# Kernel tuning notes

Measured on AMD Instinct MI355X. Metric: run time of the kernel, lower is better.

Reference implementation:

```python
import jax, jax.numpy as jnp
import numpy as np

# --- static problem geometry (compile-time constants, as in MinkowskiEngine decompositions) ---
N_TOTAL = 500000          # total points across all clouds
C = 128                   # feature channels
G = 32                    # GroupNorm groups
EPS = 1e-5                # torch GroupNorm default
LENGTHS = np.array([40000, 55000, 70000, 45000, 80000, 65000, 90000, 55000])  # points per cloud
assert LENGTHS.sum() == N_TOTAL
B = len(LENGTHS)
SEG = np.repeat(np.arange(B), LENGTHS)  # [N] cloud id for each position of the concatenated permutation


def setup_inputs() -> dict:
    key = jax.random.key(0)
    k1, k2, k3, k4 = jax.random.split(key, 4)
    feats = jax.random.normal(k1, (N_TOTAL, C), dtype=jnp.float32)   # x.F
    # concatenated decomposition_permutations: a permutation of arange(N)
    perm = jax.random.permutation(k2, N_TOTAL).astype(jnp.int64)
    gamma = 1.0 + 0.1 * jax.random.normal(k3, (C,), dtype=jnp.float32)  # GroupNorm weight
    beta = 0.1 * jax.random.normal(k4, (C,), dtype=jnp.float32)         # GroupNorm bias
    return {"feats": feats, "gamma": gamma, "beta": beta, "perm": perm}


def reference(feats, gamma, beta, perm):
    Cg = C // G
    seg = jnp.asarray(SEG)                              # [N]
    x = feats[perm]                                     # [N, C] per-cloud gather (concatenated)
    xg = x.reshape(-1, G, Cg)                           # [N, G, Cg]
    # per-(cloud, group) statistics over all points of the cloud and channels of the group
    s = jax.ops.segment_sum(xg.sum(-1), seg, num_segments=B)            # [B, G]
    ss = jax.ops.segment_sum((xg * xg).sum(-1), seg, num_segments=B)    # [B, G]
    cnt = jnp.asarray(LENGTHS * Cg, dtype=feats.dtype)[:, None]          # [B, 1]
    mean = s / cnt
    var = ss / cnt - mean * mean
    inv = jax.lax.rsqrt(var + EPS)                      # [B, G]
    xn = (xg - mean[seg][:, :, None]) * inv[seg][:, :, None]             # [N, G, Cg]
    y = xn.reshape(-1, C) * gamma + beta                # [N, C] affine per channel
    # scatter back via inverse permutation: out[perm[i]] = y[i]
    out = jnp.zeros_like(y).at[perm].set(y)
    return out
```

## Files before the change

kernel.cpp:

```cpp
#include <hip/hip_runtime.h>

#define N_TOTAL 500000
#define C 128
#define G 32
#define NB 8
#define EPS 1e-5f
#define NBLK 2048
#define RPB ((N_TOTAL + NBLK - 1) / NBLK)

typedef float f4 __attribute__((ext_vector_type(4)));

__device__ __forceinline__ int cloud_of(int i) {
    int c = 0;
    c += (i >= 40000);
    c += (i >= 95000);
    c += (i >= 165000);
    c += (i >= 210000);
    c += (i >= 290000);
    c += (i >= 355000);
    c += (i >= 445000);
    return c;
}

__device__ const float d_cnt[NB] = {160000.f, 220000.f, 280000.f, 180000.f,
                                    320000.f, 260000.f, 360000.f, 220000.f};


__global__ __launch_bounds__(256) void gn_prep(const int* __restrict__ perm,
                                               unsigned char* __restrict__ cid,
                                               float* __restrict__ ws) {
    int gid = blockIdx.x * 256 + threadIdx.x;
    if (gid < 2 * NB * G) ws[gid] = 0.f;
    for (int i = gid; i < N_TOTAL; i += 512 * 256)
        cid[perm[i]] = (unsigned char)cloud_of(i);
}

#define ACCUM(v, cl)                                                          \
    do {                                                                      \
        float rs_ = (v).x + (v).y + (v).z + (v).w;                            \
        float rss_ = (v).x * (v).x + (v).y * (v).y + (v).z * (v).z +          \
                     (v).w * (v).w;                                           \
        _Pragma("unroll")                                                     \
        for (int b = 0; b < NB; b++)                                          \
            if ((cl) == b) { s[b] += rs_; ss[b] += rss_; }                    \
    } while (0)

__global__ __launch_bounds__(256) void gn_stats(const float* __restrict__ feats,
                                                const unsigned char* __restrict__ cid,
                                                float* __restrict__ ws) {
    __shared__ float lacc[2 * NB * G];
    int tid = threadIdx.x;
    for (int k = tid; k < 2 * NB * G; k += 256) lacc[k] = 0.f;
    __syncthreads();

    const int g = tid & 31;
    const int rsub = tid >> 5;
    int start = blockIdx.x * RPB;
    int end = start + RPB;
    if (end > N_TOTAL) end = N_TOTAL;

    float s[NB], ss[NB];
#pragma unroll
    for (int b = 0; b < NB; b++) { s[b] = 0.f; ss[b] = 0.f; }

    int row = start + rsub;
    for (; row + 24 < end; row += 32) {
        int c0 = cid[row], c1 = cid[row + 8], c2 = cid[row + 16], c3 = cid[row + 24];
        f4 v0 = ((const f4*)(feats + ((long long)(row)      << 7)))[g];
        f4 v1 = ((const f4*)(feats + ((long long)(row + 8)  << 7)))[g];
        f4 v2 = ((const f4*)(feats + ((long long)(row + 16) << 7)))[g];
        f4 v3 = ((const f4*)(feats + ((long long)(row + 24) << 7)))[g];
        ACCUM(v0, c0); ACCUM(v1, c1); ACCUM(v2, c2); ACCUM(v3, c3);
    }
    for (; row < end; row += 8) {
        int c0 = cid[row];
        f4 v0 = ((const f4*)(feats + ((long long)row << 7)))[g];
        ACCUM(v0, c0);
    }

#pragma unroll
    for (int b = 0; b < NB; b++) {
        if (s[b] != 0.f || ss[b] != 0.f) {
            atomicAdd(&lacc[b * G + g], s[b]);
            atomicAdd(&lacc[NB * G + b * G + g], ss[b]);
        }
    }
    __syncthreads();

    for (int k = tid; k < 2 * NB * G; k += 256) {
        float a = lacc[k];
        if (a != 0.f) atomicAdd(&ws[k], a);
    }
}

__global__ __launch_bounds__(256) void gn_apply(const float* __restrict__ feats,
                                                const unsigned char* __restrict__ cid,
                                                const float* __restrict__ gamma,
                                                const float* __restrict__ beta,
                                                const float* __restrict__ ws,
                                                float* __restrict__ out) {
    __shared__ float lmean[NB * G];
    __shared__ float linv[NB * G];
    int tid = threadIdx.x;
    {
        float sm = ws[tid];
        float sq = ws[NB * G + tid];
        float cnt = d_cnt[tid >> 5];
        float m = sm / cnt;
        float var = sq / cnt - m * m;
        lmean[tid] = m;
        linv[tid] = rsqrtf(var + EPS);
    }
    __syncthreads();

    const int g = tid & 31;
    const int rsub = tid >> 5;
    f4 gm = ((const f4*)gamma)[g];
    f4 bt = ((const f4*)beta)[g];

    int start = blockIdx.x * RPB;
    int end = start + RPB;
    if (end > N_TOTAL) end = N_TOTAL;

#define NORM1(v, cl, r)                                                       \
    do {                                                                      \
        float m_ = lmean[(cl) * G + g];                                       \
        float i_ = linv[(cl) * G + g];                                        \
        f4 y_;                                                                \
        y_.x = ((v).x - m_) * i_ * gm.x + bt.x;                               \
        y_.y = ((v).y - m_) * i_ * gm.y + bt.y;                               \
        y_.z = ((v).z - m_) * i_ * gm.z + bt.z;                               \
        y_.w = ((v).w - m_) * i_ * gm.w + bt.w;                               \
        __builtin_nontemporal_store(y_, (f4*)(out + ((long long)(r) << 7)) + g); \
    } while (0)

    int row = start + rsub;
    for (; row + 24 < end; row += 32) {
        int c0 = cid[row], c1 = cid[row + 8], c2 = cid[row + 16], c3 = cid[row + 24];
        f4 v0 = ((const f4*)(feats + ((long long)(row)      << 7)))[g];
        f4 v1 = ((const f4*)(feats + ((long long)(row + 8)  << 7)))[g];
        f4 v2 = ((const f4*)(feats + ((long long)(row + 16) << 7)))[g];
        f4 v3 = ((const f4*)(feats + ((long long)(row + 24) << 7)))[g];
        NORM1(v0, c0, row);
        NORM1(v1, c1, row + 8);
        NORM1(v2, c2, row + 16);
        NORM1(v3, c3, row + 24);
    }
    for (; row < end; row += 8) {
        int c0 = cid[row];
        f4 v0 = ((const f4*)(feats + ((long long)row << 7)))[g];
        NORM1(v0, c0, row);
    }
#undef NORM1
}

extern "C" void kernel_launch(void* const* d_in, const int* in_sizes, int n_in,
                              void* d_out, int out_size, void* d_ws, size_t ws_size,
                              hipStream_t stream) {
    const float* feats = (const float*)d_in[0];
    const float* gamma = (const float*)d_in[1];
    const float* beta  = (const float*)d_in[2];
    const int*   perm  = (const int*)d_in[3];
    float* out = (float*)d_out;
    float* ws  = (float*)d_ws;
    unsigned char* cid = (unsigned char*)d_ws + 4096;

    gn_prep<<<512, 256, 0, stream>>>(perm, cid, ws);
    gn_stats<<<NBLK, 256, 0, stream>>>(feats, cid, ws);
    gn_apply<<<NBLK, 256, 0, stream>>>(feats, cid, gamma, beta, ws, out);
}
```

Before: 174.1 us.

## Fuse stats and apply into one cooperative kernel with hierarchical grid barrier

Merges the statistics and normalisation kernels into a single cooperative launch that uses a two-level atomic counter barrier between the reduction and apply phases. The goal is to save a kernel launch and let the second read of each block's rows hit in cache, since the same block rereads them right after the barrier. In exchange it relies on all 2048 blocks being co-resident (launch bounds of 8 waves per SIMD) and pays spin-wait cost at the barrier. If the cooperative launch fails, it falls back to the two separate kernels.

```diff
diff --git a/kernel.cpp b/kernel.cpp
--- a/kernel.cpp
+++ b/kernel.cpp
@@ -5,8 +5,10 @@
 #define G 32
 #define NB 8
 #define EPS 1e-5f
-#define NBLK 2048
-#define RPB ((N_TOTAL + NBLK - 1) / NBLK)
+#define NBLOCKS 2048
+#define RPB ((N_TOTAL + NBLOCKS - 1) / NBLOCKS)
+#define NCTR 64
+#define BLK_PER_CTR (NBLOCKS / NCTR)
 
 typedef float f4 __attribute__((ext_vector_type(4)));
 
@@ -25,15 +27,10 @@
 __device__ const float d_cnt[NB] = {160000.f, 220000.f, 280000.f, 180000.f,
                                     320000.f, 260000.f, 360000.f, 220000.f};
 
-
-__global__ __launch_bounds__(256) void gn_prep(const int* __restrict__ perm,
-                                               unsigned char* __restrict__ cid,
-                                               float* __restrict__ ws) {
-    int gid = blockIdx.x * 256 + threadIdx.x;
-    if (gid < 2 * NB * G) ws[gid] = 0.f;
-    for (int i = gid; i < N_TOTAL; i += 512 * 256)
-        cid[perm[i]] = (unsigned char)cloud_of(i);
-}
+#define CTR_OFF   (2048 / 4)
+#define ROOT_OFF  (10240 / 4)
+#define FLAG_OFF  (10368 / 4)
+#define CID_OFF   16384
 
 #define ACCUM(v, cl)                                                          \
     do {                                                                      \
@@ -45,19 +42,31 @@
             if ((cl) == b) { s[b] += rs_; ss[b] += rss_; }                    \
     } while (0)
 
-__global__ __launch_bounds__(256) void gn_stats(const float* __restrict__ feats,
-                                                const unsigned char* __restrict__ cid,
-                                                float* __restrict__ ws) {
-    __shared__ float lacc[2 * NB * G];
-    int tid = threadIdx.x;
-    for (int k = tid; k < 2 * NB * G; k += 256) lacc[k] = 0.f;
-    __syncthreads();
-
+__global__ __launch_bounds__(256) void gn_prep(const int* __restrict__ perm,
+                                               int* __restrict__ wsi,
+                                               unsigned char* __restrict__ cid) {
+    int gid = blockIdx.x * 256 + threadIdx.x;
+    if (gid < 10496 / 4) wsi[gid] = 0;
+    for (int i = gid; i < N_TOTAL; i += 512 * 256)
+        cid[perm[i]] = (unsigned char)cloud_of(i);
+}
+
+__global__ __launch_bounds__(256, 8) void gn_fused(const float* __restrict__ feats,
+                                                   const float* __restrict__ gamma,
+                                                   const float* __restrict__ beta,
+                                                   float* __restrict__ ws,
+                                                   const unsigned char* __restrict__ cid,
+                                                   float* __restrict__ out) {
+    const int tid = threadIdx.x;
     const int g = tid & 31;
     const int rsub = tid >> 5;
     int start = blockIdx.x * RPB;
     int end = start + RPB;
     if (end > N_TOTAL) end = N_TOTAL;
+
+    __shared__ float lacc[2 * NB * G];
+    for (int k = tid; k < 2 * NB * G; k += 256) lacc[k] = 0.f;
+    __syncthreads();
 
     float s[NB], ss[NB];
 #pragma unroll
@@ -91,14 +100,121 @@
         float a = lacc[k];
         if (a != 0.f) atomicAdd(&ws[k], a);
     }
-}
-
-__global__ __launch_bounds__(256) void gn_apply(const float* __restrict__ feats,
-                                                const unsigned char* __restrict__ cid,
-                                                const float* __restrict__ gamma,
-                                                const float* __restrict__ beta,
-                                                const float* __restrict__ ws,
-                                                float* __restrict__ out) {
+
+    __threadfence();
+    __syncthreads();
+    int* ctr  = (int*)ws + CTR_OFF;
+    int* root = (int*)ws + ROOT_OFF;
+    int* flag = (int*)ws + FLAG_OFF;
+    if (tid == 0) {
+        int line = (blockIdx.x & (NCTR - 1)) * 32;
+        int a = __hip_atomic_fetch_add(&ctr[line], 1, __ATOMIC_ACQ_REL,
+                                       __HIP_MEMORY_SCOPE_AGENT);
+        if (a == BLK_PER_CTR - 1) {
+            int r = __hip_atomic_fetch_add(root, 1, __ATOMIC_ACQ_REL,
+                                           __HIP_MEMORY_SCOPE_AGENT);
+            if (r == NCTR - 1) {
+                __hip_atomic_store(flag, 1, __ATOMIC_RELEASE,
+                                   __HIP_MEMORY_SCOPE_AGENT);
+            }
+        }
+        while (__hip_atomic_load(flag, __ATOMIC_ACQUIRE,
+                                 __HIP_MEMORY_SCOPE_AGENT) == 0) {
+            __builtin_amdgcn_s_sleep(8);
+        }
+    }
+    __syncthreads();
+
+    __shared__ float lmean[NB * G];
+    __shared__ float linv[NB * G];
+    {
+        float sm = __hip_atomic_load(&ws[tid], __ATOMIC_RELAXED,
+                                     __HIP_MEMORY_SCOPE_AGENT);
+        float sq = __hip_atomic_load(&ws[NB * G + tid], __ATOMIC_RELAXED,
+                                     __HIP_MEMORY_SCOPE_AGENT);
+        float cnt = d_cnt[tid >> 5];
+        float m = sm / cnt;
+        float var = sq / cnt - m * m;
+        lmean[tid] = m;
+        linv[tid] = rsqrtf(var + EPS);
+    }
+    __syncthreads();
+
+    f4 gm = ((const f4*)gamma)[g];
+    f4 bt = ((const f4*)beta)[g];
+
+#define NORM1(v, cl, r)                                                       \
+    do {                                                                      \
+        float m_ = lmean[(cl) * G + g];                                       \
+        float i_ = linv[(cl) * G + g];                                        \
+        f4 y_;                                                                \
+        y_.x = ((v).x - m_) * i_ * gm.x + bt.x;                               \
+        y_.y = ((v).y - m_) * i_ * gm.y + bt.y;                               \
+        y_.z = ((v).z - m_) * i_ * gm.z + bt.z;                               \
+        y_.w = ((v).w - m_) * i_ * gm.w + bt.w;                               \
+        __builtin_nontemporal_store(y_, (f4*)(out + ((long long)(r) << 7)) + g); \
+    } while (0)
+
+    row = start + rsub;
+    for (; row + 24 < end; row += 32) {
+        int c0 = cid[row], c1 = cid[row + 8], c2 = cid[row + 16], c3 = cid[row + 24];
+        f4 v0 = ((const f4*)(feats + ((long long)(row)      << 7)))[g];
+        f4 v1 = ((const f4*)(feats + ((long long)(row + 8)  << 7)))[g];
+        f4 v2 = ((const f4*)(feats + ((long long)(row + 16) << 7)))[g];
+        f4 v3 = ((const f4*)(feats + ((long long)(row + 24) << 7)))[g];
+        NORM1(v0, c0, row);
+        NORM1(v1, c1, row + 8);
+        NORM1(v2, c2, row + 16);
+        NORM1(v3, c3, row + 24);
+    }
+    for (; row < end; row += 8) {
+        int c0 = cid[row];
+        f4 v0 = ((const f4*)(feats + ((long long)row << 7)))[g];
+        NORM1(v0, c0, row);
+    }
+#undef NORM1
+}
+
+__global__ __launch_bounds__(256) void gn_stats_fb(const float* __restrict__ feats,
+                                                   const unsigned char* __restrict__ cid,
+                                                   float* __restrict__ ws) {
+    __shared__ float lacc[2 * NB * G];
+    int tid = threadIdx.x;
+    for (int k = tid; k < 2 * NB * G; k += 256) lacc[k] = 0.f;
+    __syncthreads();
+    const int g = tid & 31;
+    const int rsub = tid >> 5;
+    int start = blockIdx.x * RPB;
+    int end = start + RPB;
+    if (end > N_TOTAL) end = N_TOTAL;
+    float s[NB], ss[NB];
+#pragma unroll
+    for (int b = 0; b < NB; b++) { s[b] = 0.f; ss[b] = 0.f; }
+    for (int row = start + rsub; row < end; row += 8) {
+        int c0 = cid[row];
+        f4 v0 = ((const f4*)(feats + ((long long)row << 7)))[g];
+        ACCUM(v0, c0);
+    }
+#pragma unroll
+    for (int b = 0; b < NB; b++) {
+        if (s[b] != 0.f || ss[b] != 0.f) {
+            atomicAdd(&lacc[b * G + g], s[b]);
+            atomicAdd(&lacc[NB * G + b * G + g], ss[b]);
+        }
+    }
+    __syncthreads();
+    for (int k = tid; k < 2 * NB * G; k += 256) {
+        float a = lacc[k];
+        if (a != 0.f) atomicAdd(&ws[k], a);
+    }
+}
+
+__global__ __launch_bounds__(256) void gn_apply_fb(const float* __restrict__ feats,
+                                                   const unsigned char* __restrict__ cid,
+                                                   const float* __restrict__ gamma,
+                                                   const float* __restrict__ beta,
+                                                   const float* __restrict__ ws,
+                                                   float* __restrict__ out) {
     __shared__ float lmean[NB * G];
     __shared__ float linv[NB * G];
     int tid = threadIdx.x;
@@ -112,46 +228,25 @@
         linv[tid] = rsqrtf(var + EPS);
     }
     __syncthreads();
-
     const int g = tid & 31;
     const int rsub = tid >> 5;
     f4 gm = ((const f4*)gamma)[g];
     f4 bt = ((const f4*)beta)[g];
-
     int start = blockIdx.x * RPB;
     int end = start + RPB;
     if (end > N_TOTAL) end = N_TOTAL;
-
-#define NORM1(v, cl, r)                                                       \
-    do {                                                                      \
-        float m_ = lmean[(cl) * G + g];                                       \
-        float i_ = linv[(cl) * G + g];                                        \
-        f4 y_;                                                                \
-        y_.x = ((v).x - m_) * i_ * gm.x + bt.x;                               \
-        y_.y = ((v).y - m_) * i_ * gm.y + bt.y;                               \
-        y_.z = ((v).z - m_) * i_ * gm.z + bt.z;                               \
-        y_.w = ((v).w - m_) * i_ * gm.w + bt.w;                               \
-        __builtin_nontemporal_store(y_, (f4*)(out + ((long long)(r) << 7)) + g); \
-    } while (0)
-
-    int row = start + rsub;
-    for (; row + 24 < end; row += 32) {
-        int c0 = cid[row], c1 = cid[row + 8], c2 = cid[row + 16], c3 = cid[row + 24];
-        f4 v0 = ((const f4*)(feats + ((long long)(row)      << 7)))[g];
-        f4 v1 = ((const f4*)(feats + ((long long)(row + 8)  << 7)))[g];
-        f4 v2 = ((const f4*)(feats + ((long long)(row + 16) << 7)))[g];
-        f4 v3 = ((const f4*)(feats + ((long long)(row + 24) << 7)))[g];
-        NORM1(v0, c0, row);
-        NORM1(v1, c1, row + 8);
-        NORM1(v2, c2, row + 16);
-        NORM1(v3, c3, row + 24);
-    }
-    for (; row < end; row += 8) {
-        int c0 = cid[row];
-        f4 v0 = ((const f4*)(feats + ((long long)row << 7)))[g];
-        NORM1(v0, c0, row);
-    }
-#undef NORM1
+    for (int row = start + rsub; row < end; row += 8) {
+        int cl = cid[row];
+        f4 v = ((const f4*)(feats + ((long long)row << 7)))[g];
+        float m = lmean[cl * G + g];
+        float inv = linv[cl * G + g];
+        f4 y;
+        y.x = (v.x - m) * inv * gm.x + bt.x;
+        y.y = (v.y - m) * inv * gm.y + bt.y;
+        y.z = (v.z - m) * inv * gm.z + bt.z;
+        y.w = (v.w - m) * inv * gm.w + bt.w;
+        __builtin_nontemporal_store(y, (f4*)(out + ((long long)row << 7)) + g);
+    }
 }
 
 extern "C" void kernel_launch(void* const* d_in, const int* in_sizes, int n_in,
@@ -163,9 +258,17 @@
     const int*   perm  = (const int*)d_in[3];
     float* out = (float*)d_out;
     float* ws  = (float*)d_ws;
-    unsigned char* cid = (unsigned char*)d_ws + 4096;
-
-    gn_prep<<<512, 256, 0, stream>>>(perm, cid, ws);
-    gn_stats<<<NBLK, 256, 0, stream>>>(feats, cid, ws);
-    gn_apply<<<NBLK, 256, 0, stream>>>(feats, cid, gamma, beta, ws, out);
-}
+    unsigned char* cid = (unsigned char*)d_ws + CID_OFF;
+
+    gn_prep<<<512, 256, 0, stream>>>(perm, (int*)d_ws, cid);
+
+    void* args[] = {(void*)&feats, (void*)&gamma, (void*)&beta,
+                    (void*)&ws, (void*)&cid, (void*)&out};
+    hipError_t err = hipLaunchCooperativeKernel((const void*)gn_fused,
+                                                dim3(NBLOCKS), dim3(256),
+                                                args, 0, stream);
+    if (err != hipSuccess) {
+        gn_stats_fb<<<NBLOCKS, 256, 0, stream>>>(feats, cid, ws);
+        gn_apply_fb<<<NBLOCKS, 256, 0, stream>>>(feats, cid, gamma, beta, ws, out);
+    }
+}
```

New measurement: 541.3 us. 3.11x slower.

## Replace cloud-id scatter prep with direct permuted gather in stats and apply

Applied to the files above, without the earlier changes.

Removes the prep kernel that scattered per-row cloud ids, and instead walks rows in permutation order, gathering feats[perm[i]] and writing out[perm[i]], deriving the cloud from the sorted position. The stats kernel now keeps a single running accumulator per thread, flushing on cloud change, instead of eight predicated accumulators. This eliminates a random byte scatter and cid traffic, but turns contiguous streaming reads and writes into random 512-byte row gathers and scatters and drops nontemporal stores.

```diff
diff --git a/kernel.cpp b/kernel.cpp
--- a/kernel.cpp
+++ b/kernel.cpp
@@ -26,27 +26,27 @@
                                     320000.f, 260000.f, 360000.f, 220000.f};
 
 
-__global__ __launch_bounds__(256) void gn_prep(const int* __restrict__ perm,
-                                               unsigned char* __restrict__ cid,
-                                               float* __restrict__ ws) {
-    int gid = blockIdx.x * 256 + threadIdx.x;
-    if (gid < 2 * NB * G) ws[gid] = 0.f;
-    for (int i = gid; i < N_TOTAL; i += 512 * 256)
-        cid[perm[i]] = (unsigned char)cloud_of(i);
+__global__ void gn_zero(float* __restrict__ ws) {
+    int i = threadIdx.x;
+    if (i < 2 * NB * G) ws[i] = 0.f;
 }
 
-#define ACCUM(v, cl)                                                          \
+#define PROC(r, v)                                                            \
     do {                                                                      \
-        float rs_ = (v).x + (v).y + (v).z + (v).w;                            \
-        float rss_ = (v).x * (v).x + (v).y * (v).y + (v).z * (v).z +          \
-                     (v).w * (v).w;                                           \
-        _Pragma("unroll")                                                     \
-        for (int b = 0; b < NB; b++)                                          \
-            if ((cl) == b) { s[b] += rs_; ss[b] += rss_; }                    \
+        int cl_ = cloud_of(r);                                                \
+        if (cl_ != cur) {                                                     \
+            if (cur >= 0) {                                                   \
+                atomicAdd(&lacc[cur * G + g], s);                             \
+                atomicAdd(&lacc[NB * G + cur * G + g], ss);                   \
+            }                                                                 \
+            cur = cl_; s = 0.f; ss = 0.f;                                     \
+        }                                                                     \
+        s  += (v).x + (v).y + (v).z + (v).w;                                  \
+        ss += (v).x * (v).x + (v).y * (v).y + (v).z * (v).z + (v).w * (v).w;  \
     } while (0)
 
 __global__ __launch_bounds__(256) void gn_stats(const float* __restrict__ feats,
-                                                const unsigned char* __restrict__ cid,
+                                                const int* __restrict__ perm,
                                                 float* __restrict__ ws) {
     __shared__ float lacc[2 * NB * G];
     int tid = threadIdx.x;
@@ -59,31 +59,26 @@
     int end = start + RPB;
     if (end > N_TOTAL) end = N_TOTAL;
 
-    float s[NB], ss[NB];
-#pragma unroll
-    for (int b = 0; b < NB; b++) { s[b] = 0.f; ss[b] = 0.f; }
+    float s = 0.f, ss = 0.f;
+    int cur = -1;
 
     int row = start + rsub;
     for (; row + 24 < end; row += 32) {
-        int c0 = cid[row], c1 = cid[row + 8], c2 = cid[row + 16], c3 = cid[row + 24];
-        f4 v0 = ((const f4*)(feats + ((long long)(row)      << 7)))[g];
-        f4 v1 = ((const f4*)(feats + ((long long)(row + 8)  << 7)))[g];
-        f4 v2 = ((const f4*)(feats + ((long long)(row + 16) << 7)))[g];
-        f4 v3 = ((const f4*)(feats + ((long long)(row + 24) << 7)))[g];
-        ACCUM(v0, c0); ACCUM(v1, c1); ACCUM(v2, c2); ACCUM(v3, c3);
+        int p0 = perm[row], p1 = perm[row + 8], p2 = perm[row + 16], p3 = perm[row + 24];
+        f4 v0 = ((const f4*)(feats + ((long long)p0 << 7)))[g];
+        f4 v1 = ((const f4*)(feats + ((long long)p1 << 7)))[g];
+        f4 v2 = ((const f4*)(feats + ((long long)p2 << 7)))[g];
+        f4 v3 = ((const f4*)(feats + ((long long)p3 << 7)))[g];
+        PROC(row, v0); PROC(row + 8, v1); PROC(row + 16, v2); PROC(row + 24, v3);
     }
     for (; row < end; row += 8) {
-        int c0 = cid[row];
-        f4 v0 = ((const f4*)(feats + ((long long)row << 7)))[g];
-        ACCUM(v0, c0);
+        int p0 = perm[row];
+        f4 v0 = ((const f4*)(feats + ((long long)p0 << 7)))[g];
+        PROC(row, v0);
     }
-
-#pragma unroll
-    for (int b = 0; b < NB; b++) {
-        if (s[b] != 0.f || ss[b] != 0.f) {
-            atomicAdd(&lacc[b * G + g], s[b]);
-            atomicAdd(&lacc[NB * G + b * G + g], ss[b]);
-        }
+    if (cur >= 0) {
+        atomicAdd(&lacc[cur * G + g], s);
+        atomicAdd(&lacc[NB * G + cur * G + g], ss);
     }
     __syncthreads();
 
@@ -94,7 +89,7 @@
 }
 
 __global__ __launch_bounds__(256) void gn_apply(const float* __restrict__ feats,
-                                                const unsigned char* __restrict__ cid,
+                                                const int* __restrict__ perm,
                                                 const float* __restrict__ gamma,
                                                 const float* __restrict__ beta,
                                                 const float* __restrict__ ws,
@@ -122,34 +117,35 @@
     int end = start + RPB;
     if (end > N_TOTAL) end = N_TOTAL;
 
-#define NORM1(v, cl, r)                                                       \
+#define NORM1(r, p, v)                                                        \
     do {                                                                      \
-        float m_ = lmean[(cl) * G + g];                                       \
-        float i_ = linv[(cl) * G + g];                                        \
+        int cl_ = cloud_of(r);                                                \
+        float m_ = lmean[cl_ * G + g];                                        \
+        float i_ = linv[cl_ * G + g];                                         \
         f4 y_;                                                                \
         y_.x = ((v).x - m_) * i_ * gm.x + bt.x;                               \
         y_.y = ((v).y - m_) * i_ * gm.y + bt.y;                               \
         y_.z = ((v).z - m_) * i_ * gm.z + bt.z;                               \
         y_.w = ((v).w - m_) * i_ * gm.w + bt.w;                               \
-        __builtin_nontemporal_store(y_, (f4*)(out + ((long long)(r) << 7)) + g); \
+        ((f4*)(out + ((long long)(p) << 7)))[g] = y_;                         \
     } while (0)
 
     int row = start + rsub;
     for (; row + 24 < end; row += 32) {
-        int c0 = cid[row], c1 = cid[row + 8], c2 = cid[row + 16], c3 = cid[row + 24];
-        f4 v0 = ((const f4*)(feats + ((long long)(row)      << 7)))[g];
-        f4 v1 = ((const f4*)(feats + ((long long)(row + 8)  << 7)))[g];
-        f4 v2 = ((const f4*)(feats + ((long long)(row + 16) << 7)))[g];
-        f4 v3 = ((const f4*)(feats + ((long long)(row + 24) << 7)))[g];
-        NORM1(v0, c0, row);
-        NORM1(v1, c1, row + 8);
-        NORM1(v2, c2, row + 16);
-        NORM1(v3, c3, row + 24);
+        int p0 = perm[row], p1 = perm[row + 8], p2 = perm[row + 16], p3 = perm[row + 24];
+        f4 v0 = ((const f4*)(feats + ((long long)p0 << 7)))[g];
+        f4 v1 = ((const f4*)(feats + ((long long)p1 << 7)))[g];
+        f4 v2 = ((const f4*)(feats + ((long long)p2 << 7)))[g];
+        f4 v3 = ((const f4*)(feats + ((long long)p3 << 7)))[g];
+        NORM1(row, p0, v0);
+        NORM1(row + 8, p1, v1);
+        NORM1(row + 16, p2, v2);
+        NORM1(row + 24, p3, v3);
     }
     for (; row < end; row += 8) {
-        int c0 = cid[row];
-        f4 v0 = ((const f4*)(feats + ((long long)row << 7)))[g];
-        NORM1(v0, c0, row);
+        int p0 = perm[row];
+        f4 v0 = ((const f4*)(feats + ((long long)p0 << 7)))[g];
+        NORM1(row, p0, v0);
     }
 #undef NORM1
 }
@@ -163,9 +159,8 @@
     const int*   perm  = (const int*)d_in[3];
     float* out = (float*)d_out;
     float* ws  = (float*)d_ws;
-    unsigned char* cid = (unsigned char*)d_ws + 4096;
 
-    gn_prep<<<512, 256, 0, stream>>>(perm, cid, ws);
-    gn_stats<<<NBLK, 256, 0, stream>>>(feats, cid, ws);
-    gn_apply<<<NBLK, 256, 0, stream>>>(feats, cid, gamma, beta, ws, out);
+    gn_zero<<<1, 512, 0, stream>>>(ws);
+    gn_stats<<<NBLK, 256, 0, stream>>>(feats, perm, ws);
+    gn_apply<<<NBLK, 256, 0, stream>>>(feats, perm, gamma, beta, ws, out);
 }
```

Result: faster. 170.3 us (-2.1%).
